# Kernel optimization log

Measured on AMD Instinct MI355X. Metric: run time of the kernel, lower is better.

The kernel has to match this reference:

```python
import jax, jax.numpy as jnp
import numpy as np

B, T, H, O = 256, 2048, 64, 2


def setup_inputs() -> dict:
    key = jax.random.key(0)
    ks = jax.random.split(key, 14)
    def lin(k, out_f, in_f):
        bound = np.sqrt(6.0 / (in_f + out_f))
        return jax.random.uniform(k, (out_f, in_f), jnp.float32, -bound, bound)
    return {
        "x": jax.random.normal(ks[0], (B, T, 2), jnp.float32),
        "h0": jax.random.normal(ks[1], (1, B, H), jnp.float32),
        "Wa": lin(ks[2], H, H + 1), "ba": jnp.zeros((H,), jnp.float32),
        "Wp1": lin(ks[3], H, H + 1), "bp1": jnp.zeros((H,), jnp.float32),
        "Wp2": lin(ks[4], H, H + 1), "bp2": jnp.zeros((H,), jnp.float32),
        "Wf": lin(ks[5], H, 2 * H), "bf": jnp.zeros((H,), jnp.float32),
        "Wg": lin(ks[6], H, 2 * H), "bg": jnp.zeros((H,), jnp.float32),
        "Wo": lin(ks[7], O, H), "bo": jnp.zeros((O,), jnp.float32),
    }


def reference(x, h0, Wa, ba, Wp1, bp1, Wp2, bp2, Wf, bf, Wg, bg, Wo, bo):
    # x: [B, T, 2] (I/Q), h0: [1, B, H]
    xt = jnp.swapaxes(x, 0, 1)  # [T, B, 2]

    def step(h, x_t):
        i = x_t[:, 0:1]
        q = x_t[:, 1:2]
        amp = jnp.sqrt(i * i + q * q)
        theta = jnp.arctan2(q, i)
        cos_t = jnp.cos(theta)
        sin_t = jnp.sin(theta)
        a = jnp.tanh(jnp.concatenate([h, amp], -1) @ Wa.T + ba)
        p1 = jnp.tanh(jnp.concatenate([h, cos_t], -1) @ Wp1.T + bp1)
        p2 = jnp.tanh(jnp.concatenate([h, sin_t], -1) @ Wp2.T + bp2)
        u = a * p1 * p2 * (1 - a) * (1 - p1) * (1 - p2)
        hu = jnp.concatenate([h, u], -1)
        f = jax.nn.sigmoid(hu @ Wf.T + bf)
        g = jnp.tanh(hu @ Wg.T + bg)
        h_new = f * h + (1 - f) * g
        y = h_new @ Wo.T + bo
        return h_new, y

    _, ys = jax.lax.scan(step, h0[0], xt)  # ys: [T, B, O]
    return jnp.swapaxes(ys, 0, 1)  # [B, T, O]
```

## Files before the change

### kernel.cpp

```cpp
#include <hip/hip_runtime.h>
#include <math.h>

#define BB 256
#define TT 2048
#define HH 64

typedef _Float16 half2v __attribute__((ext_vector_type(2)));
typedef __fp16  fp16v2 __attribute__((ext_vector_type(2)));
union H2I { half2v h; int i; };

#if __has_builtin(__builtin_amdgcn_rcpf)
__device__ __forceinline__ float fast_rcp(float v) { return __builtin_amdgcn_rcpf(v); }
#else
__device__ __forceinline__ float fast_rcp(float v) { return 1.0f / v; }
#endif
#if __has_builtin(__builtin_amdgcn_rsqf)
__device__ __forceinline__ float fast_rsq(float v) { return __builtin_amdgcn_rsqf(v); }
#else
__device__ __forceinline__ float fast_rsq(float v) { return rsqrtf(v); }
#endif

__device__ __forceinline__ float tanh_fast(float v) {
    float e = __expf(2.0f * v);
    return fmaf(-2.0f, fast_rcp(e + 1.0f), 1.0f);
}

__device__ __forceinline__ float sigmoid_fast(float v) {
    return fast_rcp(1.0f + __expf(-v));
}

__device__ __forceinline__ float fdot2(half2v a, half2v b, float c) {
    return __builtin_amdgcn_fdot2(a, b, c, false);
}

__device__ __forceinline__ half2v pack_pair(float a, float b) {
    fp16v2 r = __builtin_amdgcn_cvt_pkrtz(a, b);
    return __builtin_bit_cast(half2v, r);
}

__device__ __forceinline__ void pin_h2(half2v& v) {
    H2I u; u.h = v;
    asm volatile("" : "+v"(u.i));
    v = u.h;
}

__device__ __forceinline__ half2v bcast_pair(half2v v, int lane) {
    H2I u; u.h = v;
    H2I w; w.i = __builtin_amdgcn_readlane(u.i, lane);
    return w.h;
}

__device__ __forceinline__ float dpp_neighbor(float v) {
    return __int_as_float(__builtin_amdgcn_mov_dpp(__float_as_int(v), 0xB1, 0xf, 0xf, true));
}

template <int CTRL>
__device__ __forceinline__ float dpp_add_stage(float v) {
    int t = __builtin_amdgcn_update_dpp(0, __float_as_int(v), CTRL, 0xf, 0xf, true);
    return v + __int_as_float(t);
}

__device__ __forceinline__ float wave_sum_dpp(float v) {
    v = dpp_add_stage<0x111>(v);
    v = dpp_add_stage<0x112>(v);
    v = dpp_add_stage<0x114>(v);
    v = dpp_add_stage<0x118>(v);
    v = dpp_add_stage<0x142>(v);
    v = dpp_add_stage<0x143>(v);
    return v;
}

__global__ __launch_bounds__(256, 1)
void pgjanet_kernel(const float* __restrict__ x,
                    const float* __restrict__ h0,
                    const float* __restrict__ Wa,  const float* __restrict__ ba,
                    const float* __restrict__ Wp1, const float* __restrict__ bp1,
                    const float* __restrict__ Wp2, const float* __restrict__ bp2,
                    const float* __restrict__ Wf,  const float* __restrict__ bf,
                    const float* __restrict__ Wg,  const float* __restrict__ bg,
                    const float* __restrict__ Wo,  const float* __restrict__ bo,
                    float* __restrict__ out)
{
    const int b   = blockIdx.x;
    const int tid = threadIdx.x;
    const int j   = tid & 63;
    const int w   = __builtin_amdgcn_readfirstlane(tid >> 6);

    __shared__ float xs[TT * 2];
    __shared__ float ybuf[TT * 2];
    __shared__ float exch[2][5][HH];

    {
        const float* xp = x + (size_t)b * (TT * 2);
        for (int i = tid; i < TT * 2; i += 256) xs[i] = xp[i];
    }

    const float* gsrc  = (w == 0) ? Wa : (w == 1) ? Wp1 : (w == 2) ? Wp2 : Wf;
    const int    gld   = (w < 3) ? (HH + 1) : (2 * HH);
    const float* g2src = (w == 3) ? Wg : gsrc;
    const int    g2ld  = (w == 3) ? (2 * HH) : gld;

    half2v wgate[32], wgate2[32], wfuv[32], wguv[32];
#pragma unroll
    for (int m = 0; m < 32; ++m) {
        wgate[m]  = pack_pair(gsrc [j * gld  + 2 * m], gsrc [j * gld  + 2 * m + 1]);
        wgate2[m] = pack_pair(g2src[j * g2ld + 2 * m], g2src[j * g2ld + 2 * m + 1]);
        wfuv[m]   = pack_pair(Wf[j * (2 * HH) + HH + 2 * m], Wf[j * (2 * HH) + HH + 2 * m + 1]);
        wguv[m]   = pack_pair(Wg[j * (2 * HH) + HH + 2 * m], Wg[j * (2 * HH) + HH + 2 * m + 1]);
    }
#pragma unroll
    for (int m = 0; m < 32; ++m) {
        pin_h2(wgate[m]); pin_h2(wgate2[m]); pin_h2(wfuv[m]); pin_h2(wguv[m]);
    }

    const float xw   = (w == 0) ? Wa [j * (HH + 1) + HH]
                     : (w == 1) ? Wp1[j * (HH + 1) + HH]
                     : (w == 2) ? Wp2[j * (HH + 1) + HH] : 0.f;
    const float bsel = (w == 0) ? ba[j] : (w == 1) ? bp1[j] : (w == 2) ? bp2[j] : 0.f;
    const float bf_r = bf[j], bg_r = bg[j];
    const float wo0 = Wo[j], wo1 = Wo[HH + j];
    const float bo0 = bo[0], bo1 = bo[1];

    float h = h0[b * HH + j];
    float* yp = out + (size_t)b * (TT * 2);

    __syncthreads();

    float xsel;
    {
        float xi = xs[0], xq = xs[1];
        float r2 = xi * xi + xq * xq;
        float rsq = fast_rsq(r2);
        bool ok = r2 > 0.f;
        float amp = ok ? r2 * rsq : 0.f;
        float ct  = ok ? xi * rsq : 1.f;
        float st  = ok ? xq * rsq : 0.f;
        xsel = (w == 0) ? amp : (w == 1) ? ct : st;
    }

    for (int t = 0; t < TT; ++t) {
        float (*ex)[HH] = exch[t & 1];

        const int tn = (t + 1 < TT) ? (t + 1) : (TT - 1);
        float xi_n = xs[2 * tn], xq_n = xs[2 * tn + 1];
        float xsel_n;
        {
            float r2 = xi_n * xi_n + xq_n * xq_n;
            float rsq = fast_rsq(r2);
            bool ok = r2 > 0.f;
            float amp = ok ? r2 * rsq : 0.f;
            float ct  = ok ? xi_n * rsq : 1.f;
            float st  = ok ? xq_n * rsq : 0.f;
            xsel_n = (w == 0) ? amp : (w == 1) ? ct : st;
        }

        float hnbr = dpp_neighbor(h);
        half2v hp = pack_pair(h, hnbr);
        half2v sh[32];
#pragma unroll
        for (int m = 0; m < 32; ++m) sh[m] = bcast_pair(hp, 2 * m);

        float a0 = 0.f, a1 = 0.f, a2 = 0.f, a3 = 0.f;
#pragma unroll
        for (int m = 0; m < 8; ++m) {
            a0 = fdot2(sh[m],      wgate[m],      a0);
            a1 = fdot2(sh[m + 8],  wgate[m + 8],  a1);
            a2 = fdot2(sh[m + 16], wgate[m + 16], a2);
            a3 = fdot2(sh[m + 24], wgate[m + 24], a3);
        }
        float pre = (a0 + a1) + (a2 + a3);

        if (w == 3) {
            float b0 = 0.f, b1 = 0.f, b2 = 0.f, b3 = 0.f;
#pragma unroll
            for (int m = 0; m < 8; ++m) {
                b0 = fdot2(sh[m],      wgate2[m],      b0);
                b1 = fdot2(sh[m + 8],  wgate2[m + 8],  b1);
                b2 = fdot2(sh[m + 16], wgate2[m + 16], b2);
                b3 = fdot2(sh[m + 24], wgate2[m + 24], b3);
            }
            ex[3][j] = pre + bf_r;
            ex[4][j] = ((b0 + b1) + (b2 + b3)) + bg_r;
        } else {
            ex[w][j] = tanh_fast(pre + fmaf(xsel, xw, bsel));
        }

        __syncthreads();

        float av  = ex[0][j];
        float pv1 = ex[1][j];
        float pv2 = ex[2][j];
        float fh  = ex[3][j];
        float gh  = ex[4][j];
        float u = (av * (1.f - av)) * (pv1 * (1.f - pv1)) * (pv2 * (1.f - pv2));

        float unbr = dpp_neighbor(u);
        half2v upk = pack_pair(u, unbr);
        half2v su[32];
#pragma unroll
        for (int m = 0; m < 32; ++m) su[m] = bcast_pair(upk, 2 * m);

        float f0 = 0.f, f1 = 0.f, f2 = 0.f, f3 = 0.f;
        float g0 = 0.f, g1 = 0.f, g2 = 0.f, g3 = 0.f;
#pragma unroll
        for (int m = 0; m < 8; ++m) {
            f0 = fdot2(su[m],      wfuv[m],      f0);
            f1 = fdot2(su[m + 8],  wfuv[m + 8],  f1);
            f2 = fdot2(su[m + 16], wfuv[m + 16], f2);
            f3 = fdot2(su[m + 24], wfuv[m + 24], f3);
            g0 = fdot2(su[m],      wguv[m],      g0);
            g1 = fdot2(su[m + 8],  wguv[m + 8],  g1);
            g2 = fdot2(su[m + 16], wguv[m + 16], g2);
            g3 = fdot2(su[m + 24], wguv[m + 24], g3);
        }
        float f = sigmoid_fast(fh + (f0 + f1) + (f2 + f3));
        float g = tanh_fast(gh + (g0 + g1) + (g2 + g3));
        h = fmaf(f, h - g, g);

        if (w == (t & 3)) {
            float y0 = wave_sum_dpp(h * wo0);
            float y1 = wave_sum_dpp(h * wo1);
            if (j == 63) {
                ybuf[2 * t]     = y0 + bo0;
                ybuf[2 * t + 1] = y1 + bo1;
            }
        }

        xsel = xsel_n;
    }

    __syncthreads();
    {
        const float4* ys4 = reinterpret_cast<const float4*>(ybuf);
        float4*       yp4 = reinterpret_cast<float4*>(yp);
        for (int i = tid; i < TT * 2 / 4; i += 256) yp4[i] = ys4[i];
    }
}

extern "C" void kernel_launch(void* const* d_in, const int* in_sizes, int n_in,
                              void* d_out, int out_size, void* d_ws, size_t ws_size,
                              hipStream_t stream) {
    const float* x   = (const float*)d_in[0];
    const float* h0  = (const float*)d_in[1];
    const float* Wa  = (const float*)d_in[2];
    const float* ba  = (const float*)d_in[3];
    const float* Wp1 = (const float*)d_in[4];
    const float* bp1 = (const float*)d_in[5];
    const float* Wp2 = (const float*)d_in[6];
    const float* bp2 = (const float*)d_in[7];
    const float* Wf  = (const float*)d_in[8];
    const float* bf  = (const float*)d_in[9];
    const float* Wg  = (const float*)d_in[10];
    const float* bg  = (const float*)d_in[11];
    const float* Wo  = (const float*)d_in[12];
    const float* bo  = (const float*)d_in[13];
    float* out = (float*)d_out;

    pgjanet_kernel<<<dim3(BB), dim3(256), 0, stream>>>(
        x, h0, Wa, ba, Wp1, bp1, Wp2, bp2, Wf, bf, Wg, bg, Wo, bo, out);
}
```

Baseline: 1.512 ms.

## Process two batch rows per 512-thread block and pack x as fp16 in LDS

Each block now handles two batch sequences with 8 waves, halving the grid to 128 blocks, so two recurrences can interleave on one CU. The input I/Q samples are converted to packed fp16 pairs in shared memory to cut LDS footprint. This risks idling half the CUs, heavier block-wide synchronisation per step, register pressure from the tighter launch bounds, and reduced input precision.

Result: slower. 2.409 ms (+59.3%).

```diff
diff --git a/kernel.cpp b/kernel.cpp
--- a/kernel.cpp
+++ b/kernel.cpp
@@ -24,42 +24,38 @@
     float e = __expf(2.0f * v);
     return fmaf(-2.0f, fast_rcp(e + 1.0f), 1.0f);
 }
-
 __device__ __forceinline__ float sigmoid_fast(float v) {
     return fast_rcp(1.0f + __expf(-v));
 }
-
 __device__ __forceinline__ float fdot2(half2v a, half2v b, float c) {
     return __builtin_amdgcn_fdot2(a, b, c, false);
 }
-
 __device__ __forceinline__ half2v pack_pair(float a, float b) {
     fp16v2 r = __builtin_amdgcn_cvt_pkrtz(a, b);
     return __builtin_bit_cast(half2v, r);
 }
-
+__device__ __forceinline__ void unpack_pair(int v, float& a, float& b) {
+    H2I u; u.i = v;
+    a = (float)u.h.x; b = (float)u.h.y;
+}
 __device__ __forceinline__ void pin_h2(half2v& v) {
     H2I u; u.h = v;
     asm volatile("" : "+v"(u.i));
     v = u.h;
 }
-
 __device__ __forceinline__ half2v bcast_pair(half2v v, int lane) {
     H2I u; u.h = v;
     H2I w; w.i = __builtin_amdgcn_readlane(u.i, lane);
     return w.h;
 }
-
 __device__ __forceinline__ float dpp_neighbor(float v) {
     return __int_as_float(__builtin_amdgcn_mov_dpp(__float_as_int(v), 0xB1, 0xf, 0xf, true));
 }
-
 template <int CTRL>
 __device__ __forceinline__ float dpp_add_stage(float v) {
     int t = __builtin_amdgcn_update_dpp(0, __float_as_int(v), CTRL, 0xf, 0xf, true);
     return v + __int_as_float(t);
 }
-
 __device__ __forceinline__ float wave_sum_dpp(float v) {
     v = dpp_add_stage<0x111>(v);
     v = dpp_add_stage<0x112>(v);
@@ -70,7 +66,7 @@
     return v;
 }
 
-__global__ __launch_bounds__(256, 1)
+__global__ __launch_bounds__(512, 2)
 void pgjanet_kernel(const float* __restrict__ x,
                     const float* __restrict__ h0,
                     const float* __restrict__ Wa,  const float* __restrict__ ba,
@@ -81,18 +77,25 @@
                     const float* __restrict__ Wo,  const float* __restrict__ bo,
                     float* __restrict__ out)
 {
-    const int b   = blockIdx.x;
     const int tid = threadIdx.x;
     const int j   = tid & 63;
-    const int w   = __builtin_amdgcn_readfirstlane(tid >> 6);
-
-    __shared__ float xs[TT * 2];
-    __shared__ float ybuf[TT * 2];
-    __shared__ float exch[2][5][HH];
+    const int w8  = __builtin_amdgcn_readfirstlane(tid >> 6);
+    const int row = w8 >> 2;
+    const int w   = w8 & 3;
+    const int b   = 2 * blockIdx.x + row;
+
+    __shared__ int   xs16[2][TT];
+    __shared__ float ybuf[2][TT * 2];
+    __shared__ float exch[2][2][5][HH];
 
     {
-        const float* xp = x + (size_t)b * (TT * 2);
-        for (int i = tid; i < TT * 2; i += 256) xs[i] = xp[i];
+        const float2* xp2 = reinterpret_cast<const float2*>(x + (size_t)b * (TT * 2));
+        const int lt = tid & 255;
+        for (int i = lt; i < TT; i += 256) {
+            float2 v = xp2[i];
+            H2I u; u.h = pack_pair(v.x, v.y);
+            xs16[row][i] = u.i;
+        }
     }
 
     const float* gsrc  = (w == 0) ? Wa : (w == 1) ? Wp1 : (w == 2) ? Wp2 : Wf;
@@ -122,13 +125,12 @@
     const float bo0 = bo[0], bo1 = bo[1];
 
     float h = h0[b * HH + j];
-    float* yp = out + (size_t)b * (TT * 2);
 
     __syncthreads();
 
     float xsel;
     {
-        float xi = xs[0], xq = xs[1];
+        float xi, xq; unpack_pair(xs16[row][0], xi, xq);
         float r2 = xi * xi + xq * xq;
         float rsq = fast_rsq(r2);
         bool ok = r2 > 0.f;
@@ -139,12 +141,12 @@
     }
 
     for (int t = 0; t < TT; ++t) {
-        float (*ex)[HH] = exch[t & 1];
+        float (*ex)[HH] = exch[row][t & 1];
 
         const int tn = (t + 1 < TT) ? (t + 1) : (TT - 1);
-        float xi_n = xs[2 * tn], xq_n = xs[2 * tn + 1];
         float xsel_n;
         {
+            float xi_n, xq_n; unpack_pair(xs16[row][tn], xi_n, xq_n);
             float r2 = xi_n * xi_n + xq_n * xq_n;
             float rsq = fast_rsq(r2);
             bool ok = r2 > 0.f;
@@ -221,8 +223,8 @@
             float y0 = wave_sum_dpp(h * wo0);
             float y1 = wave_sum_dpp(h * wo1);
             if (j == 63) {
-                ybuf[2 * t]     = y0 + bo0;
-                ybuf[2 * t + 1] = y1 + bo1;
+                ybuf[row][2 * t]     = y0 + bo0;
+                ybuf[row][2 * t + 1] = y1 + bo1;
             }
         }
 
@@ -231,9 +233,9 @@
 
     __syncthreads();
     {
-        const float4* ys4 = reinterpret_cast<const float4*>(ybuf);
-        float4*       yp4 = reinterpret_cast<float4*>(yp);
-        for (int i = tid; i < TT * 2 / 4; i += 256) yp4[i] = ys4[i];
+        const float4* ys4 = reinterpret_cast<const float4*>(&ybuf[0][0]);
+        float4*       yp4 = reinterpret_cast<float4*>(out + (size_t)(2 * blockIdx.x) * (TT * 2));
+        for (int i = tid; i < TT; i += 512) yp4[i] = ys4[i];
     }
 }
 
@@ -256,6 +258,6 @@
     const float* bo  = (const float*)d_in[13];
     float* out = (float*)d_out;
 
-    pgjanet_kernel<<<dim3(BB), dim3(256), 0, stream>>>(
+    pgjanet_kernel<<<dim3(BB / 2), dim3(512), 0, stream>>>(
         x, h0, Wa, ba, Wp1, bp1, Wp2, bp2, Wf, bf, Wg, bg, Wo, bo, out);
 }
```

## Split Wg hidden matvec across all four waves and store x as packed fp16

Applied to the files above, without the earlier changes.

The Wg·h matvec was computed entirely by wave 3, so that wave did twice the dot-product work of the other three. Each wave now computes a 16-column slice of it, and the partial sums are combined through shared memory after the barrier. Waves 0-2 also compute s*(1-s) before writing, and the x input is staged in LDS as packed fp16 pairs. The exchange adds four extra LDS reads per step, and x loses precision in the fp16 conversion.

Measured after the change: 1.781 ms. 1.18x slower.

```diff
diff --git a/kernel.cpp b/kernel.cpp
--- a/kernel.cpp
+++ b/kernel.cpp
@@ -24,42 +24,38 @@
     float e = __expf(2.0f * v);
     return fmaf(-2.0f, fast_rcp(e + 1.0f), 1.0f);
 }
-
 __device__ __forceinline__ float sigmoid_fast(float v) {
     return fast_rcp(1.0f + __expf(-v));
 }
-
 __device__ __forceinline__ float fdot2(half2v a, half2v b, float c) {
     return __builtin_amdgcn_fdot2(a, b, c, false);
 }
-
 __device__ __forceinline__ half2v pack_pair(float a, float b) {
     fp16v2 r = __builtin_amdgcn_cvt_pkrtz(a, b);
     return __builtin_bit_cast(half2v, r);
 }
-
+__device__ __forceinline__ void unpack_pair(int v, float& a, float& b) {
+    H2I u; u.i = v;
+    a = (float)u.h.x; b = (float)u.h.y;
+}
 __device__ __forceinline__ void pin_h2(half2v& v) {
     H2I u; u.h = v;
     asm volatile("" : "+v"(u.i));
     v = u.h;
 }
-
 __device__ __forceinline__ half2v bcast_pair(half2v v, int lane) {
     H2I u; u.h = v;
     H2I w; w.i = __builtin_amdgcn_readlane(u.i, lane);
     return w.h;
 }
-
 __device__ __forceinline__ float dpp_neighbor(float v) {
     return __int_as_float(__builtin_amdgcn_mov_dpp(__float_as_int(v), 0xB1, 0xf, 0xf, true));
 }
-
 template <int CTRL>
 __device__ __forceinline__ float dpp_add_stage(float v) {
     int t = __builtin_amdgcn_update_dpp(0, __float_as_int(v), CTRL, 0xf, 0xf, true);
     return v + __int_as_float(t);
 }
-
 __device__ __forceinline__ float wave_sum_dpp(float v) {
     v = dpp_add_stage<0x111>(v);
     v = dpp_add_stage<0x112>(v);
@@ -86,32 +82,38 @@
     const int j   = tid & 63;
     const int w   = __builtin_amdgcn_readfirstlane(tid >> 6);
 
-    __shared__ float xs[TT * 2];
+    __shared__ int   xs16[TT];
     __shared__ float ybuf[TT * 2];
-    __shared__ float exch[2][5][HH];
+    __shared__ float exch[2][8][HH];
 
     {
-        const float* xp = x + (size_t)b * (TT * 2);
-        for (int i = tid; i < TT * 2; i += 256) xs[i] = xp[i];
-    }
-
-    const float* gsrc  = (w == 0) ? Wa : (w == 1) ? Wp1 : (w == 2) ? Wp2 : Wf;
-    const int    gld   = (w < 3) ? (HH + 1) : (2 * HH);
-    const float* g2src = (w == 3) ? Wg : gsrc;
-    const int    g2ld  = (w == 3) ? (2 * HH) : gld;
-
-    half2v wgate[32], wgate2[32], wfuv[32], wguv[32];
+        const float2* xp2 = reinterpret_cast<const float2*>(x + (size_t)b * (TT * 2));
+        for (int i = tid; i < TT; i += 256) {
+            float2 v = xp2[i];
+            H2I u; u.h = pack_pair(v.x, v.y);
+            xs16[i] = u.i;
+        }
+    }
+
+    const float* gsrc = (w == 0) ? Wa : (w == 1) ? Wp1 : (w == 2) ? Wp2 : Wf;
+    const int    gld  = (w < 3) ? (HH + 1) : (2 * HH);
+
+    half2v wgate[32], wgsl[8], wfuv[32], wguv[32];
 #pragma unroll
     for (int m = 0; m < 32; ++m) {
-        wgate[m]  = pack_pair(gsrc [j * gld  + 2 * m], gsrc [j * gld  + 2 * m + 1]);
-        wgate2[m] = pack_pair(g2src[j * g2ld + 2 * m], g2src[j * g2ld + 2 * m + 1]);
-        wfuv[m]   = pack_pair(Wf[j * (2 * HH) + HH + 2 * m], Wf[j * (2 * HH) + HH + 2 * m + 1]);
-        wguv[m]   = pack_pair(Wg[j * (2 * HH) + HH + 2 * m], Wg[j * (2 * HH) + HH + 2 * m + 1]);
-    }
-#pragma unroll
-    for (int m = 0; m < 32; ++m) {
-        pin_h2(wgate[m]); pin_h2(wgate2[m]); pin_h2(wfuv[m]); pin_h2(wguv[m]);
-    }
+        wgate[m] = pack_pair(gsrc[j * gld + 2 * m], gsrc[j * gld + 2 * m + 1]);
+        wfuv[m]  = pack_pair(Wf[j * (2 * HH) + HH + 2 * m], Wf[j * (2 * HH) + HH + 2 * m + 1]);
+        wguv[m]  = pack_pair(Wg[j * (2 * HH) + HH + 2 * m], Wg[j * (2 * HH) + HH + 2 * m + 1]);
+    }
+#pragma unroll
+    for (int m = 0; m < 8; ++m) {
+        const int k = 16 * w + 2 * m;
+        wgsl[m] = pack_pair(Wg[j * (2 * HH) + k], Wg[j * (2 * HH) + k + 1]);
+    }
+#pragma unroll
+    for (int m = 0; m < 32; ++m) { pin_h2(wgate[m]); pin_h2(wfuv[m]); pin_h2(wguv[m]); }
+#pragma unroll
+    for (int m = 0; m < 8; ++m)  { pin_h2(wgsl[m]); }
 
     const float xw   = (w == 0) ? Wa [j * (HH + 1) + HH]
                      : (w == 1) ? Wp1[j * (HH + 1) + HH]
@@ -126,32 +128,30 @@
 
     __syncthreads();
 
-    float xsel;
-    {
-        float xi = xs[0], xq = xs[1];
+    float xsel = 0.f;
+    if (w < 3) {
+        float xi, xq; unpack_pair(xs16[0], xi, xq);
         float r2 = xi * xi + xq * xq;
         float rsq = fast_rsq(r2);
         bool ok = r2 > 0.f;
-        float amp = ok ? r2 * rsq : 0.f;
-        float ct  = ok ? xi * rsq : 1.f;
-        float st  = ok ? xq * rsq : 0.f;
-        xsel = (w == 0) ? amp : (w == 1) ? ct : st;
+        xsel = (w == 0) ? (ok ? r2 * rsq : 0.f)
+             : (w == 1) ? (ok ? xi * rsq : 1.f)
+             :            (ok ? xq * rsq : 0.f);
     }
 
     for (int t = 0; t < TT; ++t) {
         float (*ex)[HH] = exch[t & 1];
 
         const int tn = (t + 1 < TT) ? (t + 1) : (TT - 1);
-        float xi_n = xs[2 * tn], xq_n = xs[2 * tn + 1];
-        float xsel_n;
-        {
-            float r2 = xi_n * xi_n + xq_n * xq_n;
+        float xsel_n = 0.f;
+        if (w < 3) {
+            float xi, xq; unpack_pair(xs16[tn], xi, xq);
+            float r2 = xi * xi + xq * xq;
             float rsq = fast_rsq(r2);
             bool ok = r2 > 0.f;
-            float amp = ok ? r2 * rsq : 0.f;
-            float ct  = ok ? xi_n * rsq : 1.f;
-            float st  = ok ? xq_n * rsq : 0.f;
-            xsel_n = (w == 0) ? amp : (w == 1) ? ct : st;
+            xsel_n = (w == 0) ? (ok ? r2 * rsq : 0.f)
+                   : (w == 1) ? (ok ? xi * rsq : 1.f)
+                   :            (ok ? xq * rsq : 0.f);
         }
 
         float hnbr = dpp_neighbor(h);
@@ -170,29 +170,35 @@
         }
         float pre = (a0 + a1) + (a2 + a3);
 
+        float gs0 = 0.f, gs1 = 0.f;
+        if (w == 0) {
+#pragma unroll
+            for (int m = 0; m < 4; ++m) { gs0 = fdot2(sh[m], wgsl[m], gs0); gs1 = fdot2(sh[m + 4], wgsl[m + 4], gs1); }
+        } else if (w == 1) {
+#pragma unroll
+            for (int m = 0; m < 4; ++m) { gs0 = fdot2(sh[8 + m], wgsl[m], gs0); gs1 = fdot2(sh[12 + m], wgsl[m + 4], gs1); }
+        } else if (w == 2) {
+#pragma unroll
+            for (int m = 0; m < 4; ++m) { gs0 = fdot2(sh[16 + m], wgsl[m], gs0); gs1 = fdot2(sh[20 + m], wgsl[m + 4], gs1); }
+        } else {
+#pragma unroll
+            for (int m = 0; m < 4; ++m) { gs0 = fdot2(sh[24 + m], wgsl[m], gs0); gs1 = fdot2(sh[28 + m], wgsl[m + 4], gs1); }
+        }
+
         if (w == 3) {
-            float b0 = 0.f, b1 = 0.f, b2 = 0.f, b3 = 0.f;
-#pragma unroll
-            for (int m = 0; m < 8; ++m) {
-                b0 = fdot2(sh[m],      wgate2[m],      b0);
-                b1 = fdot2(sh[m + 8],  wgate2[m + 8],  b1);
-                b2 = fdot2(sh[m + 16], wgate2[m + 16], b2);
-                b3 = fdot2(sh[m + 24], wgate2[m + 24], b3);
-            }
             ex[3][j] = pre + bf_r;
-            ex[4][j] = ((b0 + b1) + (b2 + b3)) + bg_r;
         } else {
-            ex[w][j] = tanh_fast(pre + fmaf(xsel, xw, bsel));
-        }
+            float s = tanh_fast(pre + fmaf(xsel, xw, bsel));
+            ex[w][j] = s * (1.f - s);
+        }
+        ex[4 + w][j] = gs0 + gs1;
 
         __syncthreads();
 
-        float av  = ex[0][j];
-        float pv1 = ex[1][j];
-        float pv2 = ex[2][j];
-        float fh  = ex[3][j];
-        float gh  = ex[4][j];
-        float u = (av * (1.f - av)) * (pv1 * (1.f - pv1)) * (pv2 * (1.f - pv2));
+        float e0 = ex[0][j], e1 = ex[1][j], e2 = ex[2][j];
+        float fh = ex[3][j];
+        float gh = (ex[4][j] + ex[5][j]) + (ex[6][j] + ex[7][j]);
+        float u = (e0 * e1) * e2;
 
         float unbr = dpp_neighbor(u);
         half2v upk = pack_pair(u, unbr);
@@ -214,7 +220,7 @@
             g3 = fdot2(su[m + 24], wguv[m + 24], g3);
         }
         float f = sigmoid_fast(fh + (f0 + f1) + (f2 + f3));
-        float g = tanh_fast(gh + (g0 + g1) + (g2 + g3));
+        float g = tanh_fast(gh + bg_r + (g0 + g1) + (g2 + g3));
         h = fmaf(f, h - g, g);
 
         if (w == (t & 3)) {
```
